# Kernel optimization log

Measured on AMD Instinct MI355X. Metric: run time of the kernel, lower is better.

The kernel has to match this reference:

```python
import jax, jax.numpy as jnp
import numpy as np
from jax.scipy.special import logsumexp

COST_GAMMA = 0.1
MIN_ZERO_GAMMA = 0.1
_CLIP = 1.0 - 1e-7


def setup_inputs() -> dict:
    key = jax.random.key(0)
    k1, k2, k3 = jax.random.split(key, 3)
    B, D, K = 65536, 128, 1024
    xs = jax.random.normal(k1, (B, D), dtype=jnp.float32)
    xs = xs / jnp.linalg.norm(xs, axis=-1, keepdims=True)  # points on sphere S^{D-1}
    mus = jax.random.normal(k2, (D, K), dtype=jnp.float32)  # prototype params (pre-projx)
    alphas = jax.random.uniform(k3, (K,), dtype=jnp.float32)
    return {"xs": xs, "mus": mus, "alphas": alphas}


def reference(xs, mus, alphas):
    # projx: project prototype columns onto the unit sphere
    mus_p = mus / jnp.linalg.norm(mus, axis=0, keepdims=True)  # [D, K]
    # sphere cost: half squared geodesic distance, cdist-like [B, K]
    ip = jnp.clip(xs @ mus_p, -_CLIP, _CLIP)
    costs = 0.5 * jnp.arccos(ip) ** 2 + alphas  # [B, K]
    # softmin over components via stable logsumexp
    F = COST_GAMMA * logsumexp(-costs / COST_GAMMA, axis=1)  # [B]
    # soft min(F, 0): logsumexp over stacked (F, 0) == logaddexp
    F = MIN_ZERO_GAMMA * jnp.logaddexp(-F / MIN_ZERO_GAMMA, 0.0)
    return F
```

## Files before the change

kernel.cpp:

```cpp
#include <hip/hip_runtime.h>
#include <hip/hip_bf16.h>


typedef __attribute__((ext_vector_type(8))) short short8;
typedef __attribute__((ext_vector_type(4))) float f32x4;

#define KP 1024
#define DD 128

__device__ __forceinline__ unsigned int f2bf(float f) {
  unsigned int u = __float_as_uint(f);
  return (u + 0x7FFFu + ((u >> 16) & 1u)) >> 16;
}

__global__ __launch_bounds__(256) void prep_kernel(
    const float* __restrict__ mus, const float* __restrict__ alphas,
    uint4* __restrict__ musbf_sw, float* __restrict__ w) {
  __shared__ float psum[8][32];
  __shared__ float Tt[32][129];
  __shared__ float inv_s[32];
  const int t = threadIdx.x;
  const int k0 = blockIdx.x * 32;
  const int kk = t & 31, gg = t >> 5;
  float s = 0.0f;
  for (int i = 0; i < 16; ++i) {
    float v = mus[(gg * 16 + i) * KP + k0 + kk];
    s = fmaf(v, v, s);
  }
  psum[gg][kk] = s;
  __syncthreads();
  if (t < 32) {
    float tot = 0.0f;
    for (int j = 0; j < 8; ++j) tot += psum[j][t];
    inv_s[t] = rsqrtf(tot);
    w[k0 + t] = __expf(-10.0f * alphas[k0 + t]);
  }
  for (int i = 0; i < 16; ++i) {
    int e = i * 256 + t;
    Tt[e & 31][e >> 5] = mus[(e >> 5) * KP + k0 + (e & 31)];
  }
  __syncthreads();
  #pragma unroll
  for (int i = 0; i < 2; ++i) {
    int u = i * 256 + t;
    int w0 = u >> 5, c32 = u & 31;
    int col = k0 + c32;
    float inv = inv_s[c32];
    uint4 o;
    o.x = f2bf(Tt[c32][w0 * 8 + 0] * inv) | (f2bf(Tt[c32][w0 * 8 + 1] * inv) << 16);
    o.y = f2bf(Tt[c32][w0 * 8 + 2] * inv) | (f2bf(Tt[c32][w0 * 8 + 3] * inv) << 16);
    o.z = f2bf(Tt[c32][w0 * 8 + 4] * inv) | (f2bf(Tt[c32][w0 * 8 + 5] * inv) << 16);
    o.w = f2bf(Tt[c32][w0 * 8 + 6] * inv) | (f2bf(Tt[c32][w0 * 8 + 7] * inv) << 16);
    musbf_sw[((col >> 6) << 10) + (w0 << 6) + (col & 63)] = o;
  }
}

__global__ __launch_bounds__(256, 4) void main_kernel(
    const float* __restrict__ xs, const uint4* __restrict__ musbf_sw,
    const float* __restrict__ w, float* __restrict__ out) {
  __shared__ __align__(16) unsigned short Bs[2][8192];
  const int t = threadIdx.x;
  const int wv = t >> 6, ln = t & 63, q = ln >> 4, l15 = ln & 15;

  const int row = blockIdx.x * 64 + wv * 16 + l15;
  const float4* xs4 = (const float4*)xs;
  const int base4 = row * 32 + q * 2;
  short8 afr[4];
  #pragma unroll
  for (int kkk = 0; kkk < 4; ++kkk) {
    float4 f0 = xs4[base4 + kkk * 8];
    float4 f1 = xs4[base4 + kkk * 8 + 1];
    union { short8 s; uint4 u; } a;
    a.u.x = f2bf(f0.x) | (f2bf(f0.y) << 16);
    a.u.y = f2bf(f0.z) | (f2bf(f0.w) << 16);
    a.u.z = f2bf(f1.x) | (f2bf(f1.y) << 16);
    a.u.w = f2bf(f1.z) | (f2bf(f1.w) << 16);
    afr[kkk] = a.s;
  }

  uint4 v[4];
  #pragma unroll
  for (int i = 0; i < 4; ++i) v[i] = musbf_sw[i * 256 + t];
  #pragma unroll
  for (int i = 0; i < 4; ++i) *(uint4*)&Bs[0][(i * 256 + t) * 8] = v[i];
  __syncthreads();

  float sums[4] = {0.f, 0.f, 0.f, 0.f};

  for (int cg = 0; cg < 16; ++cg) {
    if (cg < 15) {
      #pragma unroll
      for (int i = 0; i < 4; ++i)
        v[i] = musbf_sw[(cg + 1) * 1024 + i * 256 + t];
    }
    float wn[4];
    #pragma unroll
    for (int nt = 0; nt < 4; ++nt) wn[nt] = w[cg * 64 + nt * 16 + l15];

    f32x4 acc[4];
    #pragma unroll
    for (int nt = 0; nt < 4; ++nt) acc[nt] = (f32x4){0.f, 0.f, 0.f, 0.f};
    const unsigned short* bp = &Bs[cg & 1][q * 512 + l15 * 8];
    #pragma unroll
    for (int kkk = 0; kkk < 4; ++kkk)
      #pragma unroll
      for (int nt = 0; nt < 4; ++nt) {
        short8 b = *(const short8*)(bp + kkk * 2048 + nt * 128);
        acc[nt] = __builtin_amdgcn_mfma_f32_16x16x32_bf16(afr[kkk], b, acc[nt], 0, 0, 0);
      }

    #pragma unroll
    for (int nt = 0; nt < 4; ++nt)
      #pragma unroll
      for (int r = 0; r < 4; ++r) {
        float x = acc[nt][r];
        float z = fmaxf(fmaf(x, -0.5f, 0.5f), 0.0f);
        float h = fmaf(z, -3.6067376f, -2.3449500f);
        h = fmaf(z, h, -3.2975886f);
        h = fmaf(z, h, -5.1295823f);
        h = fmaf(z, h, -9.6179669f);
        h = fmaf(z, h, -28.8539008f);
        float e = __builtin_amdgcn_exp2f(z * h);
        sums[r] = fmaf(e, wn[nt], sums[r]);
      }

    if (cg < 15) {
      #pragma unroll
      for (int i = 0; i < 4; ++i)
        *(uint4*)&Bs[(cg + 1) & 1][(i * 256 + t) * 8] = v[i];
      __syncthreads();
    }
  }

  #pragma unroll
  for (int s2 = 1; s2 < 16; s2 <<= 1)
    #pragma unroll
    for (int r = 0; r < 4; ++r) sums[r] += __shfl_xor(sums[r], s2, 64);
  if (l15 == 0) {
    #pragma unroll
    for (int r = 0; r < 4; ++r)
      out[blockIdx.x * 64 + wv * 16 + q * 4 + r] = 0.1f * log1pf(1.0f / sums[r]);
  }
}

extern "C" void kernel_launch(void* const* d_in, const int* in_sizes, int n_in,
                              void* d_out, int out_size, void* d_ws, size_t ws_size,
                              hipStream_t stream) {
  const float* xs     = (const float*)d_in[0];
  const float* mus    = (const float*)d_in[1];
  const float* alphas = (const float*)d_in[2];
  float* out = (float*)d_out;

  uint4* musbf_sw = (uint4*)d_ws;
  float* w = (float*)((char*)d_ws + 16384 * sizeof(uint4));

  prep_kernel<<<KP / 32, 256, 0, stream>>>(mus, alphas, musbf_sw, w);
  const int B = in_sizes[0] / DD;
  main_kernel<<<B / 64, 256, 0, stream>>>(xs, musbf_sw, w, out);
}
```

Measured before the change: 110.2 us.

## Drop LDS staging, load B fragments from global in MFMA order with register double-buffering

Prep now writes the normalized bf16 prototypes in the exact per-lane fragment order the MFMA needs. The main kernel therefore loads B fragments straight from global (L2-resident) into registers, double-buffered in two sets, with no shared memory and no barriers. Each wave now handles 32 rows (two M tiles) and reuses each B fragment across both, which halves B traffic per row; the grid is halved and launch bounds drop to 2 blocks per SM. The costs are higher register pressure and lower occupancy, and global-load latency is now hidden only by the register prefetch. The xs loads are also marked nontemporal.

```diff
diff --git a/kernel.cpp b/kernel.cpp
--- a/kernel.cpp
+++ b/kernel.cpp
@@ -15,7 +15,7 @@
 
 __global__ __launch_bounds__(256) void prep_kernel(
     const float* __restrict__ mus, const float* __restrict__ alphas,
-    uint4* __restrict__ musbf_sw, float* __restrict__ w) {
+    uint4* __restrict__ bsw, float* __restrict__ w) {
   __shared__ float psum[8][32];
   __shared__ float Tt[32][129];
   __shared__ float inv_s[32];
@@ -43,103 +43,115 @@
   #pragma unroll
   for (int i = 0; i < 2; ++i) {
     int u = i * 256 + t;
-    int w0 = u >> 5, c32 = u & 31;
-    int col = k0 + c32;
+    int c32 = u & 31, w0 = u >> 5;
     float inv = inv_s[c32];
     uint4 o;
     o.x = f2bf(Tt[c32][w0 * 8 + 0] * inv) | (f2bf(Tt[c32][w0 * 8 + 1] * inv) << 16);
     o.y = f2bf(Tt[c32][w0 * 8 + 2] * inv) | (f2bf(Tt[c32][w0 * 8 + 3] * inv) << 16);
     o.z = f2bf(Tt[c32][w0 * 8 + 4] * inv) | (f2bf(Tt[c32][w0 * 8 + 5] * inv) << 16);
     o.w = f2bf(Tt[c32][w0 * 8 + 6] * inv) | (f2bf(Tt[c32][w0 * 8 + 7] * inv) << 16);
-    musbf_sw[((col >> 6) << 10) + (w0 << 6) + (col & 63)] = o;
+    int idx = blockIdx.x * 512 + ((c32 >> 4) << 8) + ((w0 >> 2) << 6) +
+              ((w0 & 3) << 4) + (c32 & 15);
+    bsw[idx] = o;
   }
 }
 
-__global__ __launch_bounds__(256, 4) void main_kernel(
-    const float* __restrict__ xs, const uint4* __restrict__ musbf_sw,
+__global__ __launch_bounds__(256, 2) void main_kernel(
+    const float* __restrict__ xs, const uint4* __restrict__ bsw,
     const float* __restrict__ w, float* __restrict__ out) {
-  __shared__ __align__(16) unsigned short Bs[2][8192];
   const int t = threadIdx.x;
   const int wv = t >> 6, ln = t & 63, q = ln >> 4, l15 = ln & 15;
+  const int row0 = (blockIdx.x * 4 + wv) * 32;
 
-  const int row = blockIdx.x * 64 + wv * 16 + l15;
-  const float4* xs4 = (const float4*)xs;
-  const int base4 = row * 32 + q * 2;
-  short8 afr[4];
+  short8 afr[2][4];
   #pragma unroll
-  for (int kkk = 0; kkk < 4; ++kkk) {
-    float4 f0 = xs4[base4 + kkk * 8];
-    float4 f1 = xs4[base4 + kkk * 8 + 1];
-    union { short8 s; uint4 u; } a;
-    a.u.x = f2bf(f0.x) | (f2bf(f0.y) << 16);
-    a.u.y = f2bf(f0.z) | (f2bf(f0.w) << 16);
-    a.u.z = f2bf(f1.x) | (f2bf(f1.y) << 16);
-    a.u.w = f2bf(f1.z) | (f2bf(f1.w) << 16);
-    afr[kkk] = a.s;
-  }
+  for (int mt = 0; mt < 2; ++mt)
+    #pragma unroll
+    for (int kkk = 0; kkk < 4; ++kkk) {
+      const f32x4* p = (const f32x4*)(xs +
+          (size_t)(row0 + mt * 16 + l15) * DD + kkk * 32 + q * 8);
+      f32x4 f0 = __builtin_nontemporal_load(p);
+      f32x4 f1 = __builtin_nontemporal_load(p + 1);
+      union { short8 s; uint4 u; } a;
+      a.u.x = f2bf(f0.x) | (f2bf(f0.y) << 16);
+      a.u.y = f2bf(f0.z) | (f2bf(f0.w) << 16);
+      a.u.z = f2bf(f1.x) | (f2bf(f1.y) << 16);
+      a.u.w = f2bf(f1.z) | (f2bf(f1.w) << 16);
+      afr[mt][kkk] = a.s;
+    }
 
-  uint4 v[4];
+  float sums[8];
   #pragma unroll
-  for (int i = 0; i < 4; ++i) v[i] = musbf_sw[i * 256 + t];
-  #pragma unroll
-  for (int i = 0; i < 4; ++i) *(uint4*)&Bs[0][(i * 256 + t) * 8] = v[i];
-  __syncthreads();
+  for (int i = 0; i < 8; ++i) sums[i] = 0.0f;
 
-  float sums[4] = {0.f, 0.f, 0.f, 0.f};
+  const uint4* bp = bsw + ln;
 
-  for (int cg = 0; cg < 16; ++cg) {
-    if (cg < 15) {
+  short8 bA[2][4], bB[2][4];
+  auto load_b = [&](short8 bf[2][4], int j) {
+    #pragma unroll
+    for (int nt = 0; nt < 2; ++nt)
       #pragma unroll
-      for (int i = 0; i < 4; ++i)
-        v[i] = musbf_sw[(cg + 1) * 1024 + i * 256 + t];
-    }
-    float wn[4];
+      for (int kkk = 0; kkk < 4; ++kkk) {
+        union { short8 s; uint4 u; } tmp;
+        tmp.u = bp[(j * 8 + nt * 4 + kkk) * 64];
+        bf[nt][kkk] = tmp.s;
+      }
+  };
+  auto compute = [&](short8 bf[2][4], int j) {
+    float wn[2];
+    wn[0] = w[j * 32 + l15];
+    wn[1] = w[j * 32 + 16 + l15];
+    f32x4 acc[2][2];
     #pragma unroll
-    for (int nt = 0; nt < 4; ++nt) wn[nt] = w[cg * 64 + nt * 16 + l15];
-
-    f32x4 acc[4];
-    #pragma unroll
-    for (int nt = 0; nt < 4; ++nt) acc[nt] = (f32x4){0.f, 0.f, 0.f, 0.f};
-    const unsigned short* bp = &Bs[cg & 1][q * 512 + l15 * 8];
+    for (int mt = 0; mt < 2; ++mt)
+      #pragma unroll
+      for (int nt = 0; nt < 2; ++nt)
+        acc[mt][nt] = (f32x4){0.f, 0.f, 0.f, 0.f};
     #pragma unroll
     for (int kkk = 0; kkk < 4; ++kkk)
       #pragma unroll
-      for (int nt = 0; nt < 4; ++nt) {
-        short8 b = *(const short8*)(bp + kkk * 2048 + nt * 128);
-        acc[nt] = __builtin_amdgcn_mfma_f32_16x16x32_bf16(afr[kkk], b, acc[nt], 0, 0, 0);
-      }
+      for (int mt = 0; mt < 2; ++mt)
+        #pragma unroll
+        for (int nt = 0; nt < 2; ++nt)
+          acc[mt][nt] = __builtin_amdgcn_mfma_f32_16x16x32_bf16(
+              afr[mt][kkk], bf[nt][kkk], acc[mt][nt], 0, 0, 0);
+    #pragma unroll
+    for (int mt = 0; mt < 2; ++mt)
+      #pragma unroll
+      for (int nt = 0; nt < 2; ++nt)
+        #pragma unroll
+        for (int r = 0; r < 4; ++r) {
+          float x = acc[mt][nt][r];
+          float z = fmaxf(fmaf(x, -0.5f, 0.5f), 0.0f);
+          float h = fmaf(z, -3.6067376f, -2.3449500f);
+          h = fmaf(z, h, -3.2975886f);
+          h = fmaf(z, h, -5.1295823f);
+          h = fmaf(z, h, -9.6179669f);
+          h = fmaf(z, h, -28.8539008f);
+          float e = __builtin_amdgcn_exp2f(z * h);
+          sums[mt * 4 + r] = fmaf(e, wn[nt], sums[mt * 4 + r]);
+        }
+  };
 
-    #pragma unroll
-    for (int nt = 0; nt < 4; ++nt)
-      #pragma unroll
-      for (int r = 0; r < 4; ++r) {
-        float x = acc[nt][r];
-        float z = fmaxf(fmaf(x, -0.5f, 0.5f), 0.0f);
-        float h = fmaf(z, -3.6067376f, -2.3449500f);
-        h = fmaf(z, h, -3.2975886f);
-        h = fmaf(z, h, -5.1295823f);
-        h = fmaf(z, h, -9.6179669f);
-        h = fmaf(z, h, -28.8539008f);
-        float e = __builtin_amdgcn_exp2f(z * h);
-        sums[r] = fmaf(e, wn[nt], sums[r]);
-      }
-
-    if (cg < 15) {
-      #pragma unroll
-      for (int i = 0; i < 4; ++i)
-        *(uint4*)&Bs[(cg + 1) & 1][(i * 256 + t) * 8] = v[i];
-      __syncthreads();
-    }
+  load_b(bA, 0);
+  for (int j = 0; j < 32; j += 2) {
+    load_b(bB, j + 1);
+    compute(bA, j);
+    load_b(bA, (j + 2 < 32) ? (j + 2) : 31);
+    compute(bB, j + 1);
   }
 
   #pragma unroll
   for (int s2 = 1; s2 < 16; s2 <<= 1)
     #pragma unroll
-    for (int r = 0; r < 4; ++r) sums[r] += __shfl_xor(sums[r], s2, 64);
+    for (int r = 0; r < 8; ++r) sums[r] += __shfl_xor(sums[r], s2, 64);
   if (l15 == 0) {
     #pragma unroll
-    for (int r = 0; r < 4; ++r)
-      out[blockIdx.x * 64 + wv * 16 + q * 4 + r] = 0.1f * log1pf(1.0f / sums[r]);
+    for (int mt = 0; mt < 2; ++mt)
+      #pragma unroll
+      for (int r = 0; r < 4; ++r)
+        out[row0 + mt * 16 + q * 4 + r] =
+            0.1f * log1pf(1.0f / sums[mt * 4 + r]);
   }
 }
 
@@ -151,10 +163,10 @@
   const float* alphas = (const float*)d_in[2];
   float* out = (float*)d_out;
 
-  uint4* musbf_sw = (uint4*)d_ws;
+  uint4* bsw = (uint4*)d_ws;
   float* w = (float*)((char*)d_ws + 16384 * sizeof(uint4));
 
-  prep_kernel<<<KP / 32, 256, 0, stream>>>(mus, alphas, musbf_sw, w);
+  prep_kernel<<<KP / 32, 256, 0, stream>>>(mus, alphas, bsw, w);
   const int B = in_sizes[0] / DD;
-  main_kernel<<<B / 64, 256, 0, stream>>>(xs, musbf_sw, w, out);
+  main_kernel<<<B / 128, 256, 0, stream>>>(xs, bsw, w, out);
 }
```

New measurement: 116.2 us. 5.4% more time.
